# Performance work log

Hardware: AMD Instinct MI355X
Metric: run time of the kernel (lower is better)

## Reference

```python
import jax, jax.numpy as jnp
import numpy as np

GROUPS = 32
EPS = 1e-6


def group_norm(x, scale, bias):
    B, C, H, W = x.shape
    xg = x.reshape(B, GROUPS, C // GROUPS, H, W)
    mean = xg.mean(axis=(2, 3, 4), keepdims=True)
    var = xg.var(axis=(2, 3, 4), keepdims=True)
    xg = (xg - mean) * jax.lax.rsqrt(var + EPS)
    x = xg.reshape(B, C, H, W)
    return x * scale[None, :, None, None] + bias[None, :, None, None]


def conv1x1(x, w, b):
    # x: [B,C,H,W], w: [O,C], b: [O]
    return jnp.einsum('bchw,oc->bohw', x, w) + b[None, :, None, None]


def setup_inputs() -> dict:
    key = jax.random.key(0)
    ks = jax.random.split(key, 6)
    B, C, H, W = 8, 256, 64, 64
    s = 1.0 / np.sqrt(C)
    return {
        'x': jax.random.normal(ks[0], (B, C, H, W), dtype=jnp.float32),
        'gn_scale': jnp.ones((C,), dtype=jnp.float32),
        'gn_bias': jnp.zeros((C,), dtype=jnp.float32),
        'wq': jax.random.normal(ks[1], (C, C), dtype=jnp.float32) * s,
        'bq': jnp.zeros((C,), dtype=jnp.float32),
        'wk': jax.random.normal(ks[2], (C, C), dtype=jnp.float32) * s,
        'bk': jnp.zeros((C,), dtype=jnp.float32),
        'wv': jax.random.normal(ks[3], (C, C), dtype=jnp.float32) * s,
        'bv': jnp.zeros((C,), dtype=jnp.float32),
        'wo': jax.random.normal(ks[4], (C, C), dtype=jnp.float32) * s,
        'bo': jnp.zeros((C,), dtype=jnp.float32),
    }


def reference(x, gn_scale, gn_bias, wq, bq, wk, bk, wv, bv, wo, bo):
    skip = x
    h = group_norm(x, gn_scale, gn_bias)
    B, C, H, W = h.shape
    N = H * W
    q = conv1x1(h, wq, bq).reshape(B, C, N)  # [B,C,N]
    k = conv1x1(h, wk, bk).reshape(B, C, N)
    v = conv1x1(h, wv, bv).reshape(B, C, N)
    # scores[b,i,j] = sum_c q[b,c,i] k[b,c,j] / sqrt(C)
    scores = jnp.einsum('bci,bcj->bij', q, k) / jnp.sqrt(jnp.float32(C))
    a = jax.nn.softmax(scores, axis=2)  # softmax over keys j
    # z[b,c,i] = sum_j v[b,c,j] a[b,i,j]
    z = jnp.einsum('bcj,bij->bci', v, a).reshape(B, C, H, W)
    z = conv1x1(z, wo, bo)
    return skip + z
```

## Files before the change

kernel.cpp:

```cpp
#include <hip/hip_runtime.h>
#include <math.h>

typedef __bf16 bf16;
typedef __bf16 bf16x8 __attribute__((ext_vector_type(8)));
typedef __bf16 bf16x4 __attribute__((ext_vector_type(4)));
typedef float  f32x4  __attribute__((ext_vector_type(4)));
typedef float  f32x16 __attribute__((ext_vector_type(16)));
typedef unsigned int u32;
typedef unsigned char u8;
typedef u32 u32x2 __attribute__((ext_vector_type(2)));
typedef u32 u32x4 __attribute__((ext_vector_type(4)));
typedef int  i32x8 __attribute__((ext_vector_type(8)));

#define MFMA(a, b, c)   __builtin_amdgcn_mfma_f32_16x16x32_bf16((a), (b), (c), 0, 0, 0)
#define MFMAS(a, b, c)                                                           \
  __builtin_amdgcn_mfma_scale_f32_32x32x64_f8f6f4((a), (b), (c), 0, 0,           \
                                                  0, 0x7f7f7f7f, 0, 0x7f7f7f7f)

#define GLOAD_LDS16(g, l)                                                        \
  __builtin_amdgcn_global_load_lds(                                              \
      (const __attribute__((address_space(1))) void*)(g),                        \
      (__attribute__((address_space(3))) void*)(l), 16, 0, 0)

static constexpr int B_ = 8, C_ = 256, N_ = 4096;
static constexpr float QSCALE = 0.09016844005556021f;
static constexpr float PBIAS  = 2.0f;

static constexpr size_t HT_OFF = 0;
static constexpr size_t QT_OFF = 16777216;
static constexpr size_t KT_OFF = 25165824;
static constexpr size_t V_OFF  = 33554432;
static constexpr size_t WQ_OFF = 41943040;
static constexpr size_t WK_OFF = WQ_OFF + 131072;
static constexpr size_t WV_OFF = WK_OFF + 131072;
static constexpr size_t WO_OFF = WV_OFF + 131072;
static constexpr size_t LS_OFF = WO_OFF + 131072;
static constexpr size_t ZN2_OFF = LS_OFF + 524288;
static constexpr size_t PART_ELEMS = (size_t)B_ * C_ * N_;

__global__ __launch_bounds__(256) void wconv_kernel(
    const float* __restrict__ wq, const float* __restrict__ wk,
    const float* __restrict__ wv, const float* __restrict__ wo,
    bf16* __restrict__ oq, bf16* __restrict__ ok, bf16* __restrict__ ov, bf16* __restrict__ oo) {
  int i = blockIdx.x * 256 + threadIdx.x;
  oq[i] = (bf16)wq[i];
  ok[i] = (bf16)wk[i];
  ov[i] = (bf16)wv[i];
  oo[i] = (bf16)wo[i];
}

__global__ __launch_bounds__(512) void gn_kernel(
    const float* __restrict__ x, const float* __restrict__ gsc, const float* __restrict__ gbi,
    bf16* __restrict__ hT) {
  int b = blockIdx.x >> 5, g = blockIdx.x & 31, c0 = g * 8;
  int t = threadIdx.x;
  const float* base = x + ((size_t)(b * C_ + c0)) * N_;
  __shared__ bf16 xl[32768];
  float s = 0.f, ss = 0.f;
  const f32x4* b4 = (const f32x4*)base;
#pragma unroll
  for (int p = 0; p < 16; p++) {
    int u = t + p * 512;
    f32x4 v = b4[u];
    s  += v[0] + v[1] + v[2] + v[3];
    ss += v[0] * v[0] + v[1] * v[1] + v[2] * v[2] + v[3] * v[3];
    bf16x4 xv;
#pragma unroll
    for (int e = 0; e < 4; e++) xv[e] = (bf16)v[e];
    *(bf16x4*)(xl + u * 4) = xv;
  }
#pragma unroll
  for (int off = 1; off < 64; off <<= 1) {
    s  += __shfl_xor(s, off);
    ss += __shfl_xor(ss, off);
  }
  __shared__ float red[16];
  if ((t & 63) == 0) { red[(t >> 6) * 2] = s; red[(t >> 6) * 2 + 1] = ss; }
  __syncthreads();
  s = 0.f; ss = 0.f;
#pragma unroll
  for (int r = 0; r < 8; r++) { s += red[r * 2]; ss += red[r * 2 + 1]; }
  float mean = s * (1.f / 32768.f);
  float var  = ss * (1.f / 32768.f) - mean * mean;
  float rstd = rsqrtf(var + 1e-6f);
  float aa[8], bb[8];
#pragma unroll
  for (int cc = 0; cc < 8; cc++) {
    aa[cc] = rstd * gsc[c0 + cc];
    bb[cc] = gbi[c0 + cc] - mean * aa[cc];
  }
#pragma unroll
  for (int ii = 0; ii < 8; ii++) {
    int i = t + ii * 512;
    bf16x8 o;
#pragma unroll
    for (int cc = 0; cc < 8; cc++) o[cc] = (bf16)((float)xl[cc * 4096 + i] * aa[cc] + bb[cc]);
    *(bf16x8*)(hT + ((size_t)(b * N_ + i)) * C_ + c0) = o;
  }
}

__global__ __launch_bounds__(256) void qkv_kernel(
    const bf16* __restrict__ hT,
    const bf16* __restrict__ wqb, const bf16* __restrict__ wkb, const bf16* __restrict__ wvb,
    const float* __restrict__ bq, const float* __restrict__ bk, const float* __restrict__ bv,
    u8* __restrict__ qT8, u8* __restrict__ kT8, u8* __restrict__ v8) {
  int b = blockIdx.x >> 6, i0 = (blockIdx.x & 63) << 6;
  int t = threadIdx.x, w = t >> 6, lane = t & 63, quad = lane >> 4, l15 = lane & 15;
  __shared__ bf16 hl[64 * 264];
#pragma unroll
  for (int p = 0; p < 8; p++) {
    int u = t + p * 256, r = u >> 5, c16 = u & 31;
    *(bf16x8*)(hl + r * 264 + c16 * 8) =
        *(const bf16x8*)(hT + ((size_t)(b * N_ + i0 + r)) * C_ + c16 * 8);
  }
  __syncthreads();
  int cw0 = w * 64;

  f32x4 aq[4][4], ak[4][4];
#pragma unroll
  for (int a = 0; a < 4; a++)
#pragma unroll
    for (int bb2 = 0; bb2 < 4; bb2++) { aq[a][bb2] = (f32x4){0.f,0.f,0.f,0.f}; ak[a][bb2] = (f32x4){0.f,0.f,0.f,0.f}; }
  for (int kc = 0; kc < 8; kc++) {
    bf16x8 hb[4];
#pragma unroll
    for (int it = 0; it < 4; it++)
      hb[it] = *(const bf16x8*)(hl + (it * 16 + l15) * 264 + kc * 32 + quad * 8);
#pragma unroll
    for (int ct = 0; ct < 4; ct++) {
      bf16x8 wqf = *(const bf16x8*)(wqb + ((size_t)(cw0 + ct * 16 + l15)) * C_ + kc * 32 + quad * 8);
      bf16x8 wkf = *(const bf16x8*)(wkb + ((size_t)(cw0 + ct * 16 + l15)) * C_ + kc * 32 + quad * 8);
#pragma unroll
      for (int it = 0; it < 4; it++) {
        aq[ct][it] = MFMA(wqf, hb[it], aq[ct][it]);
        ak[ct][it] = MFMA(wkf, hb[it], ak[ct][it]);
      }
    }
  }
#pragma unroll
  for (int ct = 0; ct < 4; ct++)
#pragma unroll
    for (int it = 0; it < 4; it++) {
      int c4 = cw0 + ct * 16 + quad * 4;
      int i  = i0 + it * 16 + l15;
      f32x4 bq4 = *(const f32x4*)(bq + c4);
      f32x4 bk4 = *(const f32x4*)(bk + c4);
      float qv[4], kv[4];
#pragma unroll
      for (int r = 0; r < 4; r++) {
        qv[r] = (aq[ct][it][r] + bq4[r]) * (QSCALE * 4.0f);
        kv[r] = (ak[ct][it][r] + bk4[r]) * 0.25f;
      }
      u32 qd = (u32)__builtin_amdgcn_cvt_pk_fp8_f32(qv[0], qv[1], 0, false);
      qd = (u32)__builtin_amdgcn_cvt_pk_fp8_f32(qv[2], qv[3], (int)qd, true);
      u32 kd = (u32)__builtin_amdgcn_cvt_pk_fp8_f32(kv[0], kv[1], 0, false);
      kd = (u32)__builtin_amdgcn_cvt_pk_fp8_f32(kv[2], kv[3], (int)kd, true);
      *(u32*)(qT8 + ((size_t)(b * N_ + i)) * C_ + c4) = qd;
      *(u32*)(kT8 + ((size_t)(b * N_ + i)) * C_ + c4) = kd;
    }

  f32x4 av[4][4];
#pragma unroll
  for (int a = 0; a < 4; a++)
#pragma unroll
    for (int bb2 = 0; bb2 < 4; bb2++) av[a][bb2] = (f32x4){0.f,0.f,0.f,0.f};
  for (int kc = 0; kc < 8; kc++) {
    bf16x8 ha[4];
#pragma unroll
    for (int it = 0; it < 4; it++)
      ha[it] = *(const bf16x8*)(hl + (it * 16 + l15) * 264 + kc * 32 + quad * 8);
#pragma unroll
    for (int ct = 0; ct < 4; ct++) {
      bf16x8 wvf = *(const bf16x8*)(wvb + ((size_t)(cw0 + ct * 16 + l15)) * C_ + kc * 32 + quad * 8);
#pragma unroll
      for (int it = 0; it < 4; it++) av[it][ct] = MFMA(ha[it], wvf, av[it][ct]);
    }
  }
#pragma unroll
  for (int it = 0; it < 4; it++)
#pragma unroll
    for (int ct = 0; ct < 4; ct++) {
      int c  = cw0 + ct * 16 + l15;
      int i4 = i0 + it * 16 + quad * 4;
      float bvc = bv[c];
      float vv4[4];
#pragma unroll
      for (int r = 0; r < 4; r++) vv4[r] = av[it][ct][r] + bvc;
      u32 vd = (u32)__builtin_amdgcn_cvt_pk_fp8_f32(vv4[0], vv4[1], 0, false);
      vd = (u32)__builtin_amdgcn_cvt_pk_fp8_f32(vv4[2], vv4[3], (int)vd, true);
      *(u32*)(v8 + ((size_t)(b * C_ + c)) * N_ + i4) = vd;
    }
}

__global__ __launch_bounds__(256, 2) void attn_kernel(
    const u8* __restrict__ qT8, const u8* __restrict__ kT8, const u8* __restrict__ v8,
    bf16* __restrict__ zn0, bf16* __restrict__ znR, float* __restrict__ lsum) {
  constexpr int NJT = 32;
  int blk = blockIdx.x;
  int sp = blk >> 8;
  int b = blk & 7;
  int i0 = ((blk >> 3) & 31) << 7;
  int t = threadIdx.x, w = t >> 6, lane = t & 63;
  int r31 = lane & 31, h = lane >> 5;
  __shared__ __align__(16) u8 lds8[4 * 16384];

  int iw = i0 + w * 32;
  const u8* qrow = qT8 + ((size_t)(b * N_ + iw + r31)) * C_ + h * 32;
  i32x8 qB[4];
#pragma unroll
  for (int m = 0; m < 4; m++) qB[m] = *(const i32x8*)(qrow + m * 64);

  f32x16 of[8];
#pragma unroll
  for (int ct = 0; ct < 8; ct++)
#pragma unroll
    for (int e = 0; e < 16; e++) of[ct][e] = 0.f;
  float lacc = 0.f;

  int ks = r31 & 7;
  int kr_off = lane >> 4;
  int kc_pos = lane & 15;
  int vr_off = lane >> 2;
  int vc_pos = lane & 3;
  int spBase = sp * 2048;

  auto stageK = [&](int jts, u8* kb) {
    int j0s = spBase + jts * 64;
#pragma unroll
    for (int p = 0; p < 4; p++) {
      int idx = w * 4 + p;
      int r = idx * 4 + kr_off;
      int chunk = kc_pos ^ (r & 7);
      GLOAD_LDS16(kT8 + ((size_t)(b * N_ + j0s + r)) * C_ + chunk * 16, kb + idx * 1024);
    }
  };
  auto stageV = [&](int jts, u8* vb) {
    int j0s = spBase + jts * 64;
#pragma unroll
    for (int p = 0; p < 4; p++) {
      int idx = w * 4 + p;
      int c = idx * 16 + vr_off;
      int chunk = vc_pos ^ ((c >> 1) & 3);
      GLOAD_LDS16(v8 + ((size_t)(b * C_ + c)) * N_ + j0s + chunk * 16, vb + idx * 1024);
    }
  };

  stageK(0, lds8);
  stageV(0, lds8 + 32768);

  i32x8 pPrev;

  for (int jt = 0; jt < NJT; jt++) {
    stageK(jt < NJT - 1 ? jt + 1 : jt, lds8 + (((jt + 1) & 1) << 14));
    asm volatile("s_waitcnt vmcnt(8)" ::: "memory");
    __builtin_amdgcn_s_barrier();
    const u8* kTl = lds8 + ((jt & 1) << 14);
    const u8* vbp = lds8 + 32768 + (((jt + 1) & 1) << 14);

    f32x16 st0;
#pragma unroll
    for (int e = 0; e < 16; e++) st0[e] = -PBIAS;
    {
      const u8* krow = kTl + r31 * 256;
      __builtin_amdgcn_s_setprio(1);
#pragma unroll
      for (int m = 0; m < 4; m++) {
        int cd = m * 4 + h * 2;
        union { i32x8 v; u32x4 h4[2]; } kf;
        kf.h4[0] = *(const u32x4*)(krow + ((cd ^ ks) * 16));
        kf.h4[1] = *(const u32x4*)(krow + (((cd + 1) ^ ks) * 16));
        st0 = MFMAS(kf.v, qB[m], st0);
      }
    }
    if (jt) {
#pragma unroll
      for (int ct = 0; ct < 8; ct++) {
        int c = ct * 32 + r31;
        int vs = (c >> 1) & 3;
        const u8* vrow = vbp + c * 64;
        union { i32x8 v; u32x4 h4[2]; } vB;
        vB.h4[0] = *(const u32x4*)(vrow + (((2 * h) ^ vs) * 16));
        vB.h4[1] = *(const u32x4*)(vrow + (((2 * h + 1) ^ vs) * 16));
        of[ct] = MFMAS(pPrev, vB.v, of[ct]);
      }
    }
    __builtin_amdgcn_s_setprio(0);
    u32 PG0[4], PG1[4];
#pragma unroll
    for (int b4 = 0; b4 < 4; b4++) {
      float p0 = __builtin_amdgcn_exp2f(st0[b4 * 4 + 0]);
      float p1 = __builtin_amdgcn_exp2f(st0[b4 * 4 + 1]);
      float p2 = __builtin_amdgcn_exp2f(st0[b4 * 4 + 2]);
      float p3 = __builtin_amdgcn_exp2f(st0[b4 * 4 + 3]);
      lacc += (p0 + p1) + (p2 + p3);
      u32 d = (u32)__builtin_amdgcn_cvt_pk_fp8_f32(p0, p1, 0, false);
      d = (u32)__builtin_amdgcn_cvt_pk_fp8_f32(p2, p3, (int)d, true);
      PG0[b4] = d;
    }
    f32x16 st1;
#pragma unroll
    for (int e = 0; e < 16; e++) st1[e] = -PBIAS;
    {
      const u8* krow = kTl + (32 + r31) * 256;
      __builtin_amdgcn_s_setprio(1);
#pragma unroll
      for (int m = 0; m < 4; m++) {
        int cd = m * 4 + h * 2;
        union { i32x8 v; u32x4 h4[2]; } kf;
        kf.h4[0] = *(const u32x4*)(krow + ((cd ^ ks) * 16));
        kf.h4[1] = *(const u32x4*)(krow + (((cd + 1) ^ ks) * 16));
        st1 = MFMAS(kf.v, qB[m], st1);
      }
      __builtin_amdgcn_s_setprio(0);
    }
#pragma unroll
    for (int b4 = 0; b4 < 4; b4++) {
      float p0 = __builtin_amdgcn_exp2f(st1[b4 * 4 + 0]);
      float p1 = __builtin_amdgcn_exp2f(st1[b4 * 4 + 1]);
      float p2 = __builtin_amdgcn_exp2f(st1[b4 * 4 + 2]);
      float p3 = __builtin_amdgcn_exp2f(st1[b4 * 4 + 3]);
      lacc += (p0 + p1) + (p2 + p3);
      u32 d = (u32)__builtin_amdgcn_cvt_pk_fp8_f32(p0, p1, 0, false);
      d = (u32)__builtin_amdgcn_cvt_pk_fp8_f32(p2, p3, (int)d, true);
      PG1[b4] = d;
    }
#pragma unroll
    for (int b4 = 0; b4 < 4; b4++) {
      u32x2 rr = __builtin_amdgcn_permlane32_swap(PG0[b4], PG1[b4], false, false);
      pPrev[2 * b4]     = (int)rr[0];
      pPrev[2 * b4 + 1] = (int)rr[1];
    }

    __builtin_amdgcn_s_barrier();
    if (jt < NJT - 1) stageV(jt + 1, lds8 + 32768 + (((jt + 1) & 1) << 14));
  }

  asm volatile("s_waitcnt vmcnt(0)" ::: "memory");
  __builtin_amdgcn_s_barrier();
  {
    const u8* vbp = lds8 + 32768 + (((NJT - 1) & 1) << 14);
#pragma unroll
    for (int ct = 0; ct < 8; ct++) {
      int c = ct * 32 + r31;
      int vs = (c >> 1) & 3;
      const u8* vrow = vbp + c * 64;
      union { i32x8 v; u32x4 h4[2]; } vB;
      vB.h4[0] = *(const u32x4*)(vrow + (((2 * h) ^ vs) * 16));
      vB.h4[1] = *(const u32x4*)(vrow + (((2 * h + 1) ^ vs) * 16));
      of[ct] = MFMAS(pPrev, vB.v, of[ct]);
    }
  }

  lacc += __shfl_xor(lacc, 32);
  if (h == 0)
    lsum[((size_t)(sp * 8 + b)) * N_ + iw + r31] = lacc;
  bf16* zn = (sp == 0) ? zn0 : znR;
#pragma unroll
  for (int ct = 0; ct < 8; ct++) {
    int c = ct * 32 + r31;
#pragma unroll
    for (int g = 0; g < 4; g++) {
      bf16x4 zv;
#pragma unroll
      for (int e = 0; e < 4; e++) zv[e] = (bf16)of[ct][g * 4 + e];
      int i4 = iw + 8 * g + 4 * h;
      *(bf16x4*)(zn + ((size_t)(b * C_ + c)) * N_ + i4) = zv;
    }
  }
}

__global__ __launch_bounds__(256) void combine_kernel(
    const bf16* __restrict__ zn0, const bf16* __restrict__ znR,
    const float* __restrict__ lsum,
    const bf16* __restrict__ wob, const float* __restrict__ bo,
    const float* __restrict__ x, float* __restrict__ out) {
  int b = blockIdx.x >> 6, i0 = (blockIdx.x & 63) << 6;
  int t = threadIdx.x, w = t >> 6, lane = t & 63, quad = lane >> 4, l15 = lane & 15;
  __shared__ bf16 zl[64 * 264];
  __shared__ float linv[64];

  if (t < 64) {
    size_t ii = (size_t)b * N_ + i0 + t;
    linv[t] = 1.f / (lsum[ii] + lsum[ii + (size_t)8 * N_]);
  }
  __syncthreads();

#pragma unroll
  for (int p = 0; p < 16; p++) {
    int u = t + p * 256, c = u >> 4, ii = (u & 15) * 4;
    size_t base = ((size_t)(b * C_ + c)) * N_ + i0 + ii;
    bf16x4 z0 = *(const bf16x4*)(zn0 + base);
    bf16x4 z1 = *(const bf16x4*)(znR + base);
#pragma unroll
    for (int e = 0; e < 4; e++)
      zl[(ii + e) * 264 + c] = (bf16)(((float)z0[e] + (float)z1[e]) * linv[ii + e]);
  }
  __syncthreads();

  f32x4 oa[4][4];
#pragma unroll
  for (int a = 0; a < 4; a++)
#pragma unroll
    for (int bb2 = 0; bb2 < 4; bb2++) oa[a][bb2] = (f32x4){0.f, 0.f, 0.f, 0.f};
  for (int kc = 0; kc < 8; kc++) {
    bf16x8 za[4];
#pragma unroll
    for (int it = 0; it < 4; it++)
      za[it] = *(const bf16x8*)(zl + (it * 16 + l15) * 264 + kc * 32 + quad * 8);
#pragma unroll
    for (int ctl = 0; ctl < 4; ctl++) {
      bf16x8 wf = *(const bf16x8*)(wob + ((size_t)(w * 64 + ctl * 16 + l15)) * C_ + kc * 32 + quad * 8);
#pragma unroll
      for (int it = 0; it < 4; it++) oa[ctl][it] = MFMA(za[it], wf, oa[ctl][it]);
    }
  }
#pragma unroll
  for (int ctl = 0; ctl < 4; ctl++)
#pragma unroll
    for (int it = 0; it < 4; it++) {
      int c = w * 64 + ctl * 16 + l15;
      size_t base = ((size_t)(b * C_ + c)) * N_ + i0 + it * 16 + quad * 4;
      f32x4 xs = *(const f32x4*)(x + base);
      float boc = bo[c];
      f32x4 o4;
#pragma unroll
      for (int r = 0; r < 4; r++) o4[r] = oa[ctl][it][r] + boc + xs[r];
      *(f32x4*)(out + base) = o4;
    }
}

extern "C" void kernel_launch(void* const* d_in, const int* in_sizes, int n_in,
                              void* d_out, int out_size, void* d_ws, size_t ws_size,
                              hipStream_t stream) {
  const float* x   = (const float*)d_in[0];
  const float* gsc = (const float*)d_in[1];
  const float* gbi = (const float*)d_in[2];
  const float* wq  = (const float*)d_in[3];
  const float* bq  = (const float*)d_in[4];
  const float* wk  = (const float*)d_in[5];
  const float* bk  = (const float*)d_in[6];
  const float* wv  = (const float*)d_in[7];
  const float* bv  = (const float*)d_in[8];
  const float* wo  = (const float*)d_in[9];
  const float* bo  = (const float*)d_in[10];

  char* ws = (char*)d_ws;
  bf16* hT   = (bf16*)(ws + HT_OFF);
  u8*   qT8  = (u8*)(ws + QT_OFF);
  u8*   kT8  = (u8*)(ws + KT_OFF);
  u8*   v8   = (u8*)(ws + V_OFF);
  bf16* wqb  = (bf16*)(ws + WQ_OFF);
  bf16* wkb  = (bf16*)(ws + WK_OFF);
  bf16* wvb  = (bf16*)(ws + WV_OFF);
  bf16* wob  = (bf16*)(ws + WO_OFF);
  float* lsum = (float*)(ws + LS_OFF);
  bf16* zn0  = (bf16*)(ws + HT_OFF);
  bf16* znR  = (bf16*)(ws + ZN2_OFF);

  wconv_kernel<<<256, 256, 0, stream>>>(wq, wk, wv, wo, wqb, wkb, wvb, wob);
  gn_kernel<<<256, 512, 0, stream>>>(x, gsc, gbi, hT);
  qkv_kernel<<<512, 256, 0, stream>>>(hT, wqb, wkb, wvb, bq, bk, bv, qT8, kT8, v8);
  attn_kernel<<<512, 256, 0, stream>>>(qT8, kT8, v8, zn0, znR, lsum);
  combine_kernel<<<512, 256, 0, stream>>>(zn0, znR, lsum, wob, bo, x, (float*)d_out);
}
```

Before: 247.6 us.

## Software-pipeline second score tile's exp across iterations to interleave with MFMAs

The loop is restructured so the exp2/fp8 conversion of the second score half (st1) is deferred to the next iteration, where it is interleaved with the first-half QK MFMAs. The st0 exponentials are in turn interleaved with the PV MFMAs. The aim is to hide transcendental ALU latency behind matrix-core work instead of running them in serial phases. This carries st1, PG0 and pPrev across iterations, which raises register pressure, and adds an epilogue that drains the last st1 before the final PV.

```diff
diff --git a/kernel.cpp b/kernel.cpp
--- a/kernel.cpp
+++ b/kernel.cpp
@@ -249,6 +249,8 @@
   stageV(0, lds8 + 32768);
 
   i32x8 pPrev;
+  f32x16 st1;
+  u32 PG0[4];
 
   for (int jt = 0; jt < NJT; jt++) {
     stageK(jt < NJT - 1 ? jt + 1 : jt, lds8 + (((jt + 1) & 1) << 14));
@@ -257,72 +259,97 @@
     const u8* kTl = lds8 + ((jt & 1) << 14);
     const u8* vbp = lds8 + 32768 + (((jt + 1) & 1) << 14);
 
+    __builtin_amdgcn_s_setprio(1);
     f32x16 st0;
 #pragma unroll
     for (int e = 0; e < 16; e++) st0[e] = -PBIAS;
+    const u8* krow0 = kTl + r31 * 256;
+    u32 PG1[4];
+#pragma unroll
+    for (int m = 0; m < 4; m++) {
+      int cd = m * 4 + h * 2;
+      union { i32x8 v; u32x4 h4[2]; } kf;
+      kf.h4[0] = *(const u32x4*)(krow0 + ((cd ^ ks) * 16));
+      kf.h4[1] = *(const u32x4*)(krow0 + (((cd + 1) ^ ks) * 16));
+      st0 = MFMAS(kf.v, qB[m], st0);
+      if (jt) {
+        float p0 = __builtin_amdgcn_exp2f(st1[m * 4 + 0]);
+        float p1 = __builtin_amdgcn_exp2f(st1[m * 4 + 1]);
+        float p2 = __builtin_amdgcn_exp2f(st1[m * 4 + 2]);
+        float p3 = __builtin_amdgcn_exp2f(st1[m * 4 + 3]);
+        lacc += (p0 + p1) + (p2 + p3);
+        u32 d = (u32)__builtin_amdgcn_cvt_pk_fp8_f32(p0, p1, 0, false);
+        d = (u32)__builtin_amdgcn_cvt_pk_fp8_f32(p2, p3, (int)d, true);
+        PG1[m] = d;
+      }
+    }
+    if (jt) {
+#pragma unroll
+      for (int b4 = 0; b4 < 4; b4++) {
+        u32x2 rr = __builtin_amdgcn_permlane32_swap(PG0[b4], PG1[b4], false, false);
+        pPrev[2 * b4]     = (int)rr[0];
+        pPrev[2 * b4 + 1] = (int)rr[1];
+      }
+    }
+
+#pragma unroll
+    for (int b4 = 0; b4 < 4; b4++) {
+      if (jt) {
+#pragma unroll
+        for (int half = 0; half < 2; half++) {
+          int ct = 2 * b4 + half;
+          int c = ct * 32 + r31;
+          int vs = (c >> 1) & 3;
+          const u8* vrow = vbp + c * 64;
+          union { i32x8 v; u32x4 h4[2]; } vB;
+          vB.h4[0] = *(const u32x4*)(vrow + (((2 * h) ^ vs) * 16));
+          vB.h4[1] = *(const u32x4*)(vrow + (((2 * h + 1) ^ vs) * 16));
+          of[ct] = MFMAS(pPrev, vB.v, of[ct]);
+        }
+      }
+      {
+        float p0 = __builtin_amdgcn_exp2f(st0[b4 * 4 + 0]);
+        float p1 = __builtin_amdgcn_exp2f(st0[b4 * 4 + 1]);
+        float p2 = __builtin_amdgcn_exp2f(st0[b4 * 4 + 2]);
+        float p3 = __builtin_amdgcn_exp2f(st0[b4 * 4 + 3]);
+        lacc += (p0 + p1) + (p2 + p3);
+        u32 d = (u32)__builtin_amdgcn_cvt_pk_fp8_f32(p0, p1, 0, false);
+        d = (u32)__builtin_amdgcn_cvt_pk_fp8_f32(p2, p3, (int)d, true);
+        PG0[b4] = d;
+      }
+    }
+
+#pragma unroll
+    for (int e = 0; e < 16; e++) st1[e] = -PBIAS;
     {
-      const u8* krow = kTl + r31 * 256;
-      __builtin_amdgcn_s_setprio(1);
+      const u8* krow1 = kTl + (32 + r31) * 256;
 #pragma unroll
       for (int m = 0; m < 4; m++) {
         int cd = m * 4 + h * 2;
         union { i32x8 v; u32x4 h4[2]; } kf;
-        kf.h4[0] = *(const u32x4*)(krow + ((cd ^ ks) * 16));
-        kf.h4[1] = *(const u32x4*)(krow + (((cd + 1) ^ ks) * 16));
-        st0 = MFMAS(kf.v, qB[m], st0);
-      }
-    }
-    if (jt) {
-#pragma unroll
-      for (int ct = 0; ct < 8; ct++) {
-        int c = ct * 32 + r31;
-        int vs = (c >> 1) & 3;
-        const u8* vrow = vbp + c * 64;
-        union { i32x8 v; u32x4 h4[2]; } vB;
-        vB.h4[0] = *(const u32x4*)(vrow + (((2 * h) ^ vs) * 16));
-        vB.h4[1] = *(const u32x4*)(vrow + (((2 * h + 1) ^ vs) * 16));
-        of[ct] = MFMAS(pPrev, vB.v, of[ct]);
+        kf.h4[0] = *(const u32x4*)(krow1 + ((cd ^ ks) * 16));
+        kf.h4[1] = *(const u32x4*)(krow1 + (((cd + 1) ^ ks) * 16));
+        st1 = MFMAS(kf.v, qB[m], st1);
       }
     }
     __builtin_amdgcn_s_setprio(0);
-    u32 PG0[4], PG1[4];
-#pragma unroll
-    for (int b4 = 0; b4 < 4; b4++) {
-      float p0 = __builtin_amdgcn_exp2f(st0[b4 * 4 + 0]);
-      float p1 = __builtin_amdgcn_exp2f(st0[b4 * 4 + 1]);
-      float p2 = __builtin_amdgcn_exp2f(st0[b4 * 4 + 2]);
-      float p3 = __builtin_amdgcn_exp2f(st0[b4 * 4 + 3]);
+
+    __builtin_amdgcn_s_barrier();
+    if (jt < NJT - 1) stageV(jt + 1, lds8 + 32768 + (((jt + 1) & 1) << 14));
+  }
+
+  {
+    u32 PG1[4];
+#pragma unroll
+    for (int m = 0; m < 4; m++) {
+      float p0 = __builtin_amdgcn_exp2f(st1[m * 4 + 0]);
+      float p1 = __builtin_amdgcn_exp2f(st1[m * 4 + 1]);
+      float p2 = __builtin_amdgcn_exp2f(st1[m * 4 + 2]);
+      float p3 = __builtin_amdgcn_exp2f(st1[m * 4 + 3]);
       lacc += (p0 + p1) + (p2 + p3);
       u32 d = (u32)__builtin_amdgcn_cvt_pk_fp8_f32(p0, p1, 0, false);
       d = (u32)__builtin_amdgcn_cvt_pk_fp8_f32(p2, p3, (int)d, true);
-      PG0[b4] = d;
-    }
-    f32x16 st1;
-#pragma unroll
-    for (int e = 0; e < 16; e++) st1[e] = -PBIAS;
-    {
-      const u8* krow = kTl + (32 + r31) * 256;
-      __builtin_amdgcn_s_setprio(1);
-#pragma unroll
-      for (int m = 0; m < 4; m++) {
-        int cd = m * 4 + h * 2;
-        union { i32x8 v; u32x4 h4[2]; } kf;
-        kf.h4[0] = *(const u32x4*)(krow + ((cd ^ ks) * 16));
-        kf.h4[1] = *(const u32x4*)(krow + (((cd + 1) ^ ks) * 16));
-        st1 = MFMAS(kf.v, qB[m], st1);
-      }
-      __builtin_amdgcn_s_setprio(0);
-    }
-#pragma unroll
-    for (int b4 = 0; b4 < 4; b4++) {
-      float p0 = __builtin_amdgcn_exp2f(st1[b4 * 4 + 0]);
-      float p1 = __builtin_amdgcn_exp2f(st1[b4 * 4 + 1]);
-      float p2 = __builtin_amdgcn_exp2f(st1[b4 * 4 + 2]);
-      float p3 = __builtin_amdgcn_exp2f(st1[b4 * 4 + 3]);
-      lacc += (p0 + p1) + (p2 + p3);
-      u32 d = (u32)__builtin_amdgcn_cvt_pk_fp8_f32(p0, p1, 0, false);
-      d = (u32)__builtin_amdgcn_cvt_pk_fp8_f32(p2, p3, (int)d, true);
-      PG1[b4] = d;
+      PG1[m] = d;
     }
 #pragma unroll
     for (int b4 = 0; b4 < 4; b4++) {
@@ -330,11 +357,7 @@
       pPrev[2 * b4]     = (int)rr[0];
       pPrev[2 * b4 + 1] = (int)rr[1];
     }
-
-    __builtin_amdgcn_s_barrier();
-    if (jt < NJT - 1) stageV(jt + 1, lds8 + 32768 + (((jt + 1) & 1) << 14));
-  }
-
+  }
   asm volatile("s_waitcnt vmcnt(0)" ::: "memory");
   __builtin_amdgcn_s_barrier();
   {
```

Result: slower. 289.5 us (+16.9%).
